# Kernel tuning notes

Hardware: AMD Instinct MI355X
Metric: run time of the kernel (lower is better)

Reference implementation:

```python
import jax, jax.numpy as jnp
import numpy as np

B, S, E, H = 2, 2048, 1024, 16
Dh = E // H
LN_EPS = 1e-5


def setup_inputs() -> dict:
    key = jax.random.key(0)
    ks = jax.random.split(key, 12)
    std = 1.0 / np.sqrt(E)
    inp = {
        "query": jax.random.normal(ks[0], (B, S, E), jnp.float32),
        "key":   jax.random.normal(ks[1], (B, S, E), jnp.float32),
        "value": jax.random.normal(ks[2], (B, S, E), jnp.float32),
        # True = masked. Causal mask so every row keeps >=1 valid entry.
        "mask": jnp.broadcast_to(jnp.triu(jnp.ones((S, S), bool), k=1), (B, S, S)),
        # per-head QKV projections, stacked: weight [H, Dh, E] (torch Linear layout), bias [H, Dh]
        "Wq_w": jax.random.uniform(ks[3], (H, Dh, E), jnp.float32, -std, std),
        "Wq_b": jax.random.uniform(ks[4], (H, Dh), jnp.float32, -std, std),
        "Wk_w": jax.random.uniform(ks[5], (H, Dh, E), jnp.float32, -std, std),
        "Wk_b": jax.random.uniform(ks[6], (H, Dh), jnp.float32, -std, std),
        "Wv_w": jax.random.uniform(ks[7], (H, Dh, E), jnp.float32, -std, std),
        "Wv_b": jax.random.uniform(ks[8], (H, Dh), jnp.float32, -std, std),
        # output projection [E, E] (torch layout: out = x @ W.T + b)
        "out_w": jax.random.uniform(ks[9], (E, E), jnp.float32, -std, std),
        "out_b": jax.random.uniform(ks[10], (E,), jnp.float32, -std, std),
        "ln_g": jnp.ones((E,), jnp.float32),
        "ln_b": jnp.zeros((E,), jnp.float32),
    }
    return inp


def reference(query, key, value, mask, Wq_w, Wq_b, Wk_w, Wk_b, Wv_w, Wv_b, out_w, out_b, ln_g, ln_b):
    # per-head projections (batched over heads): [B,S,E] x [H,Dh,E] -> [B,H,S,Dh]
    q = jnp.einsum('bse,hde->bhsd', query, Wq_w) + Wq_b[None, :, None, :]
    k = jnp.einsum('bse,hde->bhsd', key,   Wk_w) + Wk_b[None, :, None, :]
    v = jnp.einsum('bse,hde->bhsd', value, Wv_w) + Wv_b[None, :, None, :]
    scale = 1.0 / np.sqrt(Dh).astype(np.float32)
    scores = jnp.einsum('bhsd,bhtd->bhst', q, k) * scale  # [B,H,S,S]
    scores = jnp.where(mask[:, None, :, :], -jnp.inf, scores)
    probs = jax.nn.softmax(scores, axis=-1)  # dropout p=0 (eval)
    ctx = jnp.einsum('bhst,bhtd->bhsd', probs, v)  # [B,H,S,Dh]
    att = ctx.transpose(0, 2, 1, 3).reshape(query.shape[0], query.shape[1], -1)  # concat heads [B,S,E]
    proj = att @ out_w.T + out_b  # dropout p=0
    x = query + proj  # residual
    mu = jnp.mean(x, axis=-1, keepdims=True)
    var = jnp.mean(jnp.square(x - mu), axis=-1, keepdims=True)
    return (x - mu) * jax.lax.rsqrt(var + LN_EPS) * ln_g + ln_b
```

## Files before the change

### kernel.cpp

```cpp
#include <hip/hip_runtime.h>
#include <stdint.h>

#define B_ 2
#define S_ 2048
#define E_ 1024
#define H_ 16
#define DH 64
#define M_TOT (B_*S_)

typedef short s16x8 __attribute__((ext_vector_type(8)));
typedef float f32x4 __attribute__((ext_vector_type(4)));
typedef unsigned int u32;
typedef unsigned short u16;

union V8 { uint4 u; s16x8 v; };

__device__ __forceinline__ u32 fbits(float f){ union{float f;u32 i;}x; x.f=f; return x.i; }
__device__ __forceinline__ u32 prround(float f){ return fbits(f)+0x8000u; }
__device__ __forceinline__ u16 f2bf(float f){ return (u16)(prround(f)>>16); }
__device__ __forceinline__ u32 permpack(u32 hi,u32 lo){ return __builtin_amdgcn_perm(hi,lo,0x07060302u); }
__device__ __forceinline__ uint4 pack8r(const float4 a, const float4 b){
    uint4 p;
    p.x = permpack(prround(a.y),prround(a.x));
    p.y = permpack(prround(a.w),prround(a.z));
    p.z = permpack(prround(b.y),prround(b.x));
    p.w = permpack(prround(b.w),prround(b.z));
    return p;
}
__device__ __forceinline__ float exp2_fast(float x){ float r; asm("v_exp_f32 %0, %1":"=v"(r):"v"(x)); return r; }

typedef const __attribute__((address_space(1))) u32* gas_t;
typedef __attribute__((address_space(3))) u32* las_t;
#define GLDS16(gp, lp) __builtin_amdgcn_global_load_lds((gas_t)(gp), (las_t)(lp), 16, 0, 0)

#define MFMA16(a,b,c) __builtin_amdgcn_mfma_f32_16x16x32_bf16((a),(b),(c),0,0,0)

__global__ __launch_bounds__(256) void cvtw(
    const float* __restrict__ w0, const float* __restrict__ w1, const float* __restrict__ w2,
    u16* __restrict__ dst, int n4)
{
    const int z = blockIdx.y;
    const float* s = (z==0)?w0:(z==1)?w1:w2;
    u16* d = dst + (size_t)z*E_*E_;
    int i = blockIdx.x*256 + threadIdx.x;
    const int stride = gridDim.x*256;
    for (; i<n4; i+=stride){
        float4 v = ((const float4*)s)[i];
        uint2 p;
        p.x = permpack(prround(v.y),prround(v.x));
        p.y = permpack(prround(v.w),prround(v.z));
        ((uint2*)d)[i] = p;
    }
}
__global__ __launch_bounds__(256) void cvt1(
    const float* __restrict__ s, u16* __restrict__ d, int n4)
{
    int i = blockIdx.x*256 + threadIdx.x;
    const int stride = gridDim.x*256;
    for (; i<n4; i+=stride){
        float4 v = ((const float4*)s)[i];
        uint2 p;
        p.x = permpack(prround(v.y),prround(v.x));
        p.y = permpack(prround(v.w),prround(v.z));
        ((uint2*)d)[i] = p;
    }
}
__global__ __launch_bounds__(256) void cvtx(
    const float* __restrict__ x0, const float* __restrict__ x1, const float* __restrict__ x2,
    u16* __restrict__ d0, u16* __restrict__ d1, u16* __restrict__ d2, int n4)
{
    const int z = blockIdx.y;
    const float* s = (z==0)?x0:(z==1)?x1:x2;
    u16* d = (z==0)?d0:(z==1)?d1:d2;
    int i = blockIdx.x*256 + threadIdx.x;
    const int stride = gridDim.x*256;
    for (; i<n4; i+=stride){
        float4 v = ((const float4*)s)[i];
        uint2 p;
        p.x = permpack(prround(v.y),prround(v.x));
        p.y = permpack(prround(v.w),prround(v.z));
        ((uint2*)d)[i] = p;
    }
}
__global__ __launch_bounds__(256) void cvtall(
    const float* __restrict__ w0, const float* __restrict__ w1, const float* __restrict__ w2,
    const float* __restrict__ ow,
    const float* __restrict__ x0, const float* __restrict__ x1, const float* __restrict__ x2,
    u16* __restrict__ wbf, u16* __restrict__ owbf,
    u16* __restrict__ dq, u16* __restrict__ dk, u16* __restrict__ dv)
{
    const int z = blockIdx.y;
    const float* s;
    u16* d;
    int n4;
    if (z < 3){ s = (z==0)?w0:(z==1)?w1:w2; d = wbf + (size_t)z*E_*E_; n4 = (E_*E_)/4; }
    else if (z == 3){ s = ow; d = owbf; n4 = (E_*E_)/4; }
    else { s = (z==4)?x0:(z==5)?x1:x2; d = (z==4)?dq:(z==5)?dk:dv; n4 = (M_TOT*E_)/4; }
    int i = blockIdx.x*256 + threadIdx.x;
    const int stride = gridDim.x*256;
    for (; i<n4; i+=stride){
        float4 v = ((const float4*)s)[i];
        uint2 p;
        p.x = permpack(prround(v.y),prround(v.x));
        p.y = permpack(prround(v.w),prround(v.z));
        ((uint2*)d)[i] = p;
    }
}

__global__ __launch_bounds__(256,3) void qkv128(
    const float* __restrict__ xv,
    const u16* __restrict__ xqb, const u16* __restrict__ xkb, const u16* __restrict__ xvb,
    const u16* __restrict__ Wb,
    const float* __restrict__ bq, const float* __restrict__ bk, const float* __restrict__ bv,
    u16* __restrict__ oq, u16* __restrict__ ok_, u16* __restrict__ ovt)
{
    const int bid = blockIdx.x;
    const int c = bid & 7;
    const int tdec = bid >> 3;
    const int n = tdec & 7;
    const int g = ((tdec >> 3) << 3) + c;
    const int m = g & 31, z = g >> 5;

    const u16* W = Wb + (size_t)z*E_*E_;
    const float* bia = (z==0)?bq:(z==1)?bk:bv;
    const float scale = (z==0)? 0.125f*1.44269504f : 1.0f;

    __shared__ __align__(16) u16 As[3][128*32];
    __shared__ __align__(16) u16 Bs[3][128*32];

    const int tid = threadIdx.x;
    const int wid = tid>>6, lane = tid&63;
    const int lrow = lane&15, quad = lane>>4;
    const int mb = m*128, nb = n*128;
    const int wm = (wid>>1)*64, wn = (wid&1)*64;
    const int srow = lane>>2, skq = lane&3;

    f32x4 acc[4][4] = {};
    const u16*  Wn = W + (size_t)nb*E_;

    auto stageB = [&](u16* Bd, int kt){
        const int k0 = kt*32;
#pragma unroll
        for (int i=0;i<2;i++){
            const int rb = wid*32 + i*16;
            GLDS16(Wn + (size_t)(rb+srow)*E_ + k0 + ((skq^(srow&3))<<3), Bd + rb*32);
        }
    };

    const u16* Abf = (z==0)? xqb : (z==1)? xkb : xvb;

    if (Abf){
        const u16* Am = Abf + (size_t)mb*E_;
        auto stageA = [&](u16* Ad, int kt){
            const int k0 = kt*32;
#pragma unroll
            for (int i=0;i<2;i++){
                const int rb = wid*32 + i*16;
                GLDS16(Am + (size_t)(rb+srow)*E_ + k0 + ((skq^(srow&3))<<3), Ad + rb*32);
            }
        };
        stageA(As[0], 0); stageB(Bs[0], 0);
        stageA(As[1], 1); stageB(Bs[1], 1);

        int tc = 0;
#pragma unroll 1
        for (int kt=0; kt<32; ++kt){
            const int ts = (kt+2 < 32) ? kt+2 : 31;
            const int tn = (tc+2 >= 3) ? tc-1 : tc+2;
            asm volatile("s_waitcnt vmcnt(4) lgkmcnt(0)" ::: "memory");
            __builtin_amdgcn_s_barrier();
            __builtin_amdgcn_sched_barrier(0);

            const u16* Ad = As[tc];
            const u16* Bd = Bs[tc];
            const int fq_ = (quad^(lrow&3))<<3;
            s16x8 a0 = *(const s16x8*)&Ad[(wm+ 0+lrow)*32 + fq_];
            s16x8 a1 = *(const s16x8*)&Ad[(wm+16+lrow)*32 + fq_];
            s16x8 a2 = *(const s16x8*)&Ad[(wm+32+lrow)*32 + fq_];
            s16x8 a3 = *(const s16x8*)&Ad[(wm+48+lrow)*32 + fq_];
            s16x8 b0 = *(const s16x8*)&Bd[(wn+ 0+lrow)*32 + fq_];
            s16x8 b1 = *(const s16x8*)&Bd[(wn+16+lrow)*32 + fq_];
            s16x8 b2 = *(const s16x8*)&Bd[(wn+32+lrow)*32 + fq_];
            s16x8 b3 = *(const s16x8*)&Bd[(wn+48+lrow)*32 + fq_];
            __builtin_amdgcn_sched_barrier(0);
            stageA(As[tn], ts);
            stageB(Bs[tn], ts);
            __builtin_amdgcn_sched_barrier(0);
            __builtin_amdgcn_s_setprio(1);
            acc[0][0] = MFMA16(a0, b0, acc[0][0]);
            acc[0][1] = MFMA16(a0, b1, acc[0][1]);
            acc[0][2] = MFMA16(a0, b2, acc[0][2]);
            acc[0][3] = MFMA16(a0, b3, acc[0][3]);
            acc[1][0] = MFMA16(a1, b0, acc[1][0]);
            acc[1][1] = MFMA16(a1, b1, acc[1][1]);
            acc[1][2] = MFMA16(a1, b2, acc[1][2]);
            acc[1][3] = MFMA16(a1, b3, acc[1][3]);
            acc[2][0] = MFMA16(a2, b0, acc[2][0]);
            acc[2][1] = MFMA16(a2, b1, acc[2][1]);
            acc[2][2] = MFMA16(a2, b2, acc[2][2]);
            acc[2][3] = MFMA16(a2, b3, acc[2][3]);
            acc[3][0] = MFMA16(a3, b0, acc[3][0]);
            acc[3][1] = MFMA16(a3, b1, acc[3][1]);
            acc[3][2] = MFMA16(a3, b2, acc[3][2]);
            acc[3][3] = MFMA16(a3, b3, acc[3][3]);
            __builtin_amdgcn_s_setprio(0);
            tc = (tc+1==3)?0:tc+1;
        }
        asm volatile("s_waitcnt vmcnt(0) lgkmcnt(0)" ::: "memory");
    } else {
        const int arow = wid*32 + (lane>>1);
        const int akh  = lane&1;
        const int ag0  = akh*2;
        const int asw  = arow&3;
        const float* Xrow = xv + (size_t)(mb+arow)*E_ + akh*16;

        float4 arA0, arA1, arA2, arA3;
        float4 arB0, arB1, arB2, arB3;

#define QKV_ISSUEA(KT, AR) do {                                   \
        const float* xp_ = Xrow + ((KT)<<5);                      \
        AR##0 = *(const float4*)(xp_    );                        \
        AR##1 = *(const float4*)(xp_ + 4);                        \
        AR##2 = *(const float4*)(xp_ + 8);                        \
        AR##3 = *(const float4*)(xp_ +12);                        \
    } while(0)

#define QKV_WRITEA(AD, AR) do {                                   \
        const uint4 w0_ = pack8r(AR##0, AR##1);                   \
        const uint4 w1_ = pack8r(AR##2, AR##3);                   \
        *(uint4*)&(AD)[arow*32 + (((ag0  )^asw)<<3)] = w0_;       \
        *(uint4*)&(AD)[arow*32 + (((ag0+1)^asw)<<3)] = w1_;       \
    } while(0)

#define QKV_ITER(KT, TC, ARC, ARN) do {                                       \
        const int ts_ = ((KT)+2 < 32) ? (KT)+2 : 31;                          \
        const int tw_ = ((TC)+1==3)?0:(TC)+1;                                 \
        const int tn_ = (tw_+1==3)?0:tw_+1;                                   \
        const u16* Ad_ = As[TC];                                              \
        const u16* Bd_ = Bs[TC];                                              \
        asm volatile("s_waitcnt vmcnt(6) lgkmcnt(0)" ::: "memory");           \
        __builtin_amdgcn_s_barrier();                                         \
        __builtin_amdgcn_sched_barrier(0);                                    \
        const int fq_ = (quad^(lrow&3))<<3;                                   \
        s16x8 a0 = *(const s16x8*)&Ad_[(wm+ 0+lrow)*32 + fq_];                \
        s16x8 a1 = *(const s16x8*)&Ad_[(wm+16+lrow)*32 + fq_];                \
        s16x8 a2 = *(const s16x8*)&Ad_[(wm+32+lrow)*32 + fq_];                \
        s16x8 a3 = *(const s16x8*)&Ad_[(wm+48+lrow)*32 + fq_];                \
        s16x8 b0 = *(const s16x8*)&Bd_[(wn+ 0+lrow)*32 + fq_];                \
        s16x8 b1 = *(const s16x8*)&Bd_[(wn+16+lrow)*32 + fq_];                \
        s16x8 b2 = *(const s16x8*)&Bd_[(wn+32+lrow)*32 + fq_];                \
        s16x8 b3 = *(const s16x8*)&Bd_[(wn+48+lrow)*32 + fq_];                \
        __builtin_amdgcn_sched_barrier(0);                                    \
        QKV_ISSUEA(ts_, ARN);                                                 \
        __builtin_amdgcn_sched_barrier(0);                                    \
        stageB(Bs[tn_], ts_);                                                 \
        __builtin_amdgcn_sched_barrier(0);                                    \
        __builtin_amdgcn_s_setprio(1);                                        \
        acc[0][0] = MFMA16(a0, b0, acc[0][0]);                                \
        acc[0][1] = MFMA16(a0, b1, acc[0][1]);                                \
        acc[0][2] = MFMA16(a0, b2, acc[0][2]);                                \
        acc[0][3] = MFMA16(a0, b3, acc[0][3]);                                \
        acc[1][0] = MFMA16(a1, b0, acc[1][0]);                                \
        acc[1][1] = MFMA16(a1, b1, acc[1][1]);                                \
        acc[1][2] = MFMA16(a1, b2, acc[1][2]);                                \
        acc[1][3] = MFMA16(a1, b3, acc[1][3]);                                \
        __builtin_amdgcn_s_setprio(0);                                        \
        QKV_WRITEA(As[tw_], ARC);                                             \
        __builtin_amdgcn_s_setprio(1);                                        \
        acc[2][0] = MFMA16(a2, b0, acc[2][0]);                                \
        acc[2][1] = MFMA16(a2, b1, acc[2][1]);                                \
        acc[2][2] = MFMA16(a2, b2, acc[2][2]);                                \
        acc[2][3] = MFMA16(a2, b3, acc[2][3]);                                \
        acc[3][0] = MFMA16(a3, b0, acc[3][0]);                                \
        acc[3][1] = MFMA16(a3, b1, acc[3][1]);                                \
        acc[3][2] = MFMA16(a3, b2, acc[3][2]);                                \
        acc[3][3] = MFMA16(a3, b3, acc[3][3]);                                \
        __builtin_amdgcn_s_setprio(0);                                        \
    } while(0)

        QKV_ISSUEA(0, arA);
        stageB(Bs[0], 0);
        QKV_WRITEA(As[0], arA);
        QKV_ISSUEA(1, arA);
        stageB(Bs[1], 1);

        int tc = 0;
#pragma unroll 1
        for (int k2=0; k2<16; ++k2){
            const int kt0 = k2*2;
            QKV_ITER(kt0,   tc, arA, arB);
            tc = (tc+1==3)?0:tc+1;
            QKV_ITER(kt0+1, tc, arB, arA);
            tc = (tc+1==3)?0:tc+1;
        }
        asm volatile("s_waitcnt vmcnt(0) lgkmcnt(0)" ::: "memory");
#undef QKV_ITER
#undef QKV_WRITEA
#undef QKV_ISSUEA
    }

    if (z < 2){
        u16* O = (z==0)?oq:ok_;
#pragma unroll
        for (int ci=0;ci<4;ci++){
            const int nn = nb+wn+ci*16+lrow;
            const float bval = bia[nn];
            const int h = nn>>6, d = nn&63;
#pragma unroll
            for (int mi=0;mi<4;mi++){
#pragma unroll
                for (int r=0;r<4;r++){
                    const int mm = mb+wm+mi*16+quad*4+r;
                    const int bb = mm>>11, s = mm&(S_-1);
                    O[(((size_t)(bb*H_+h))*S_+s)*DH + d] = f2bf((acc[mi][ci][r]+bval)*scale);
                }
            }
        }
    } else {
#pragma unroll
        for (int ci=0;ci<4;ci++){
            const int nn = nb+wn+ci*16+lrow;
            const float bval = bia[nn];
            const int h = nn>>6, d = nn&63;
#pragma unroll
            for (int mi=0;mi<4;mi++){
                const int m0 = mb+wm+mi*16+quad*4;
                const int bb = m0>>11, s0 = m0&(S_-1);
                uint2 pk;
                pk.x = permpack(prround(acc[mi][ci][1]+bval), prround(acc[mi][ci][0]+bval));
                pk.y = permpack(prround(acc[mi][ci][3]+bval), prround(acc[mi][ci][2]+bval));
                *(uint2*)&ovt[(((size_t)(bb*H_+h))*DH + d)*S_ + s0] = pk;
            }
        }
    }
}

__global__ __launch_bounds__(512,2) void attn8(
    const u16* __restrict__ q_ws, const u16* __restrict__ k_ws,
    const u16* __restrict__ vt_ws, u16* __restrict__ att)
{
    const int bid = blockIdx.x;
    const int c8 = bid & 7;
    const int t = bid >> 3;
    const int p = t & 15;
    const int bh = ((t >> 4) << 3) + c8;
    const int b = bh>>4, h = bh&15;

    const u16* Qb = q_ws + (size_t)bh*S_*DH;
    const u16* Kb = k_ws + (size_t)bh*S_*DH;
    const u16* VT = vt_ws + (size_t)bh*DH*S_;

    __shared__ __align__(16) u16 Ks[2][2][64*64];
    __shared__ __align__(16) u16 Vt[2][2][64*64];
    __shared__ __align__(16) u16 Ps[8][16*64];

    const int tid = threadIdx.x;
    const int wid = tid>>6, lane = tid&63;
    const int grp = wid>>2, w4 = wid&3;
    const int lrow = lane&15, quad = lane>>4;
    u16* Pw = Ps[wid];

    const int srw = lane>>3;
    const int scs = lane&7;
    const int sgc = scs ^ srw;

    auto stageKV = [&](u16* Kd, u16* Vd, int t0){
#pragma unroll
        for (int g2=0; g2<2; g2++){
            const int rg = w4*16 + g2*8 + srw;
            GLDS16(Kb + (size_t)(t0+rg)*DH + (sgc<<3), Kd + (w4*16+g2*8)*64);
            GLDS16(VT + (size_t)rg*S_ + t0 + (sgc<<3), Vd + (w4*16+g2*8)*64);
        }
    };

    float* oex = (float*)&Ks[0][0][0];
    float* lex = (float*)&Vt[0][0][0];

    for (int ph=0; ph<2; ph++){
        const int qi = ph ? (31-p) : p;
        const int qb = qi<<6;
        const int ntg   = (qi >= grp) ? (((qi-grp)>>1)+1) : 0;
        const int ntmax = (qi>>1)+1;

        s16x8 qf[2];
#pragma unroll
        for (int ch=0;ch<2;ch++)
            qf[ch] = *(const s16x8*)&Qb[(size_t)(qb+w4*16+lrow)*DH + ch*32 + quad*8];

        f32x4 o[4] = {};
        float l_lane = 0.f;
        const int qglob = qb + w4*16 + lrow;

        auto computeTile = [&](const u16* Kd, const u16* Vd, int t0, bool diag){
            f32x4 st[4] = {};
#pragma unroll
            for (int tt=0;tt<4;tt++){
                const int tr = tt*16+lrow;
#pragma unroll
                for (int ch=0;ch<2;ch++){
                    const int slot = (ch*4+quad) ^ (lrow&7);
                    const s16x8 kf = *(const s16x8*)&Kd[tr*64 + slot*8];
                    st[tt] = __builtin_amdgcn_mfma_f32_16x16x32_bf16(kf, qf[ch], st[tt],0,0,0);
                }
            }
            if (diag){
#pragma unroll
                for (int tt=0;tt<4;tt++){
                    const int tg = t0 + tt*16 + quad*4;
#pragma unroll
                    for (int r=0;r<4;r++)
                        if (tg + r > qglob) st[tt][r] = -1e30f;
                }
            }
#pragma unroll
            for (int tt=0;tt<4;tt++){
                const float p0 = exp2_fast(st[tt][0]);
                const float p1 = exp2_fast(st[tt][1]);
                const float p2 = exp2_fast(st[tt][2]);
                const float p3 = exp2_fast(st[tt][3]);
                l_lane += (p0+p1)+(p2+p3);
                const int tc = tt*2 + (quad>>1);
                const int ts = tc ^ (lrow&7);
                const int a0 = lrow*64 + ts*8 + (quad&1)*4;
                *(u32*)&Pw[a0]   = permpack(prround(p1),prround(p0));
                *(u32*)&Pw[a0+2] = permpack(prround(p3),prround(p2));
            }
            s16x8 pb[2];
#pragma unroll
            for (int ch=0;ch<2;ch++){
                const int slot = (ch*4+quad) ^ (lrow&7);
                pb[ch] = *(const s16x8*)&Pw[lrow*64 + slot*8];
            }
#pragma unroll
            for (int cc=0;cc<4;cc++){
                const int vr = cc*16+lrow;
#pragma unroll
                for (int ch=0;ch<2;ch++){
                    const int slot = (ch*4+quad) ^ (lrow&7);
                    const s16x8 vf = *(const s16x8*)&Vd[vr*64 + slot*8];
                    o[cc] = __builtin_amdgcn_mfma_f32_16x16x32_bf16(vf, pb[ch], o[cc],0,0,0);
                }
            }
        };

        __syncthreads();
        if (ntg > 0) stageKV(Ks[grp][0], Vt[grp][0], grp<<6);
#pragma unroll 1
        for (int i=0; i<ntmax; ++i){
            __syncthreads();
            if (i+1 < ntg) stageKV(Ks[grp][(i+1)&1], Vt[grp][(i+1)&1], (grp+2*(i+1))<<6);
            if (i < ntg){
                const int tile = grp + 2*i;
                computeTile(Ks[grp][i&1], Vt[grp][i&1], tile<<6, tile==qi);
            }
        }

        float s = l_lane;
        s += __shfl_xor(s, 16, 64);
        s += __shfl_xor(s, 32, 64);

        __syncthreads();
        if (grp == 1){
            float* dst = oex + (size_t)(w4*64 + lane)*16;
#pragma unroll
            for (int cc=0;cc<4;cc++) *(f32x4*)&dst[cc*4] = o[cc];
            if (quad == 0) lex[w4*16 + lrow] = s;
        }
        __syncthreads();
        if (grp == 0){
            const float* src = oex + (size_t)(w4*64 + lane)*16;
#pragma unroll
            for (int cc=0;cc<4;cc++) o[cc] += *(const f32x4*)&src[cc*4];
            const float rl = 1.0f/(s + lex[w4*16 + lrow]);
#pragma unroll
            for (int cc=0;cc<4;cc++){
                uint2 pk;
                pk.x = permpack(prround(o[cc][1]*rl), prround(o[cc][0]*rl));
                pk.y = permpack(prround(o[cc][3]*rl), prround(o[cc][2]*rl));
                *(uint2*)&att[(size_t)(b*S_ + qglob)*E_ + h*DH + cc*16 + quad*4] = pk;
            }
        }
    }
}

__global__ __launch_bounds__(256,4) void oproj64(
    const u16* __restrict__ A, const u16* __restrict__ W, const float* __restrict__ bias,
    const float* __restrict__ resid, float* __restrict__ out)
{
    const int bid = blockIdx.x;
    const int c = bid & 7;
    const int tdec = bid >> 3;
    const int n = tdec & 15;
    const int m = ((tdec >> 4) << 3) + c;

    __shared__ __align__(16) u16 As[3][64*32];
    __shared__ __align__(16) u16 Bs[3][64*32];

    const int tid = threadIdx.x;
    const int wid = tid>>6, lane = tid&63;
    const int lrow = lane&15, quad = lane>>4;
    const int mb = m*64, nb = n*64;
    const int wm = (wid>>1)*32, wn = (wid&1)*32;
    const int srow = lane>>2, skq = lane&3;

    f32x4 acc[2][2] = {};
    const u16* Ab = A + (size_t)mb*E_;
    const u16* Wn = W + (size_t)nb*E_;

    auto stage = [&](u16* Ad, u16* Bd, int kt){
        const int k0 = kt*32;
        const int kc = (skq^(srow&3))<<3;
        const int rb = wid*16;
        GLDS16(Ab + (size_t)(rb+srow)*E_ + k0 + kc, Ad + rb*32);
        GLDS16(Wn + (size_t)(rb+srow)*E_ + k0 + kc, Bd + rb*32);
    };

    stage(As[0], Bs[0], 0);
    stage(As[1], Bs[1], 1);

    int tc = 0, tn = 2;
#pragma unroll 1
    for (int kt=0; kt<32; ++kt){
        const int ts = (kt+2 < 32) ? kt+2 : 31;
        asm volatile("s_waitcnt vmcnt(2) lgkmcnt(0)" ::: "memory");
        __builtin_amdgcn_s_barrier();
        __builtin_amdgcn_sched_barrier(0);

        const u16* Ad = As[tc];
        const u16* Bd = Bs[tc];
        const int fq = (quad^(lrow&3))<<3;
        s16x8 a0 = *(const s16x8*)&Ad[(wm+ 0+lrow)*32 + fq];
        s16x8 a1 = *(const s16x8*)&Ad[(wm+16+lrow)*32 + fq];
        s16x8 b0 = *(const s16x8*)&Bd[(wn+ 0+lrow)*32 + fq];
        s16x8 b1 = *(const s16x8*)&Bd[(wn+16+lrow)*32 + fq];
        __builtin_amdgcn_sched_barrier(0);
        stage(As[tn], Bs[tn], ts);
        __builtin_amdgcn_sched_barrier(0);
        __builtin_amdgcn_s_setprio(1);
        acc[0][0] = MFMA16(a0, b0, acc[0][0]);
        acc[0][1] = MFMA16(a0, b1, acc[0][1]);
        acc[1][0] = MFMA16(a1, b0, acc[1][0]);
        acc[1][1] = MFMA16(a1, b1, acc[1][1]);
        __builtin_amdgcn_s_setprio(0);
        tc = (tc+1==3)?0:tc+1;
        tn = (tn+1==3)?0:tn+1;
    }
    asm volatile("s_waitcnt vmcnt(0)" ::: "memory");

#pragma unroll
    for (int ci=0;ci<2;ci++){
        const int nn = nb+wn+ci*16+lrow;
        const float bval = bias[nn];
#pragma unroll
        for (int mi=0;mi<2;mi++){
#pragma unroll
            for (int r=0;r<4;r++){
                const int mm = mb+wm+mi*16+quad*4+r;
                out[(size_t)mm*E_+nn] = acc[mi][ci][r] + bval + resid[(size_t)mm*E_+nn];
            }
        }
    }
}

__global__ __launch_bounds__(256) void ln_k(
    const float* __restrict__ xin, const float* __restrict__ lg,
    const float* __restrict__ lb, float* __restrict__ out)
{
    const int row = blockIdx.x;
    const int tid = threadIdx.x;
    const int wid = tid>>6, lane = tid&63;
    const float* xr = xin + (size_t)row*E_;

    float x[4];
    float s = 0.f;
#pragma unroll
    for (int i=0;i<4;i++){ const int e = i*256+tid; x[i] = xr[e]; s += x[i]; }
    __shared__ float red[8];
#pragma unroll
    for (int off=32; off>0; off>>=1) s += __shfl_xor(s, off, 64);
    if (lane==0) red[wid] = s;
    __syncthreads();
    const float mu = (red[0]+red[1]+red[2]+red[3]) * (1.f/E_);

    float v = 0.f;
#pragma unroll
    for (int i=0;i<4;i++){ const float d = x[i]-mu; v += d*d; }
#pragma unroll
    for (int off=32; off>0; off>>=1) v += __shfl_xor(v, off, 64);
    if (lane==0) red[wid+4] = v;
    __syncthreads();
    const float var = (red[4]+red[5]+red[6]+red[7]) * (1.f/E_);
    const float rs = rsqrtf(var + 1e-5f);

#pragma unroll
    for (int i=0;i<4;i++){
        const int e = i*256+tid;
        out[(size_t)row*E_+e] = (x[i]-mu)*rs*lg[e] + lb[e];
    }
}

extern "C" void kernel_launch(void* const* d_in, const int* in_sizes, int n_in,
                              void* d_out, int out_size, void* d_ws, size_t ws_size,
                              hipStream_t stream) {
    const float* q_in = (const float*)d_in[0];
    const float* k_in = (const float*)d_in[1];
    const float* v_in = (const float*)d_in[2];
    const float* wq = (const float*)d_in[4];
    const float* bq = (const float*)d_in[5];
    const float* wk = (const float*)d_in[6];
    const float* bk = (const float*)d_in[7];
    const float* wv = (const float*)d_in[8];
    const float* bv = (const float*)d_in[9];
    const float* ow = (const float*)d_in[10];
    const float* ob = (const float*)d_in[11];
    const float* lg = (const float*)d_in[12];
    const float* lb = (const float*)d_in[13];
    float* out = (float*)d_out;

    char* ws = (char*)d_ws;
    const size_t MB = (size_t)1<<20;
    u16* q_ws  = (u16*)(ws);
    u16* k_ws  = (u16*)(ws +  8*MB);
    u16* vt_ws = (u16*)(ws + 16*MB);
    u16* att   = (u16*)(ws + 24*MB);
    u16* Wbf   = (u16*)(ws + 24*MB);
    float* proj = (float*)ws;

    u16* xqbf = (u16*)out;
    u16* xkbf = (u16*)((char*)out + 8*MB);

    if (ws_size >= 48*MB){
        u16* xvbf = (u16*)(ws + 32*MB);
        u16* owbf = (u16*)(ws + 40*MB);

        cvtall<<<dim3(1024,7), 256, 0, stream>>>(
            wq, wk, wv, ow, q_in, k_in, v_in, Wbf, owbf, xqbf, xkbf, xvbf);
        qkv128<<<dim3(768), 256, 0, stream>>>(
            v_in, xqbf, xkbf, xvbf, Wbf, bq, bk, bv, q_ws, k_ws, vt_ws);
        attn8<<<dim3(512), 512, 0, stream>>>(q_ws, k_ws, vt_ws, att);
        oproj64<<<dim3(1024), 256, 0, stream>>>(att, owbf, ob, q_in, proj);
        ln_k<<<dim3(M_TOT), 256, 0, stream>>>(proj, lg, lb, out);
    } else {
        u16* owbf = (u16*)(ws + 16*MB);
        u16* xvbf = (ws_size >= 40*MB) ? (u16*)(ws + 32*MB) : (u16*)0;

        cvtw<<<dim3(512,3), 256, 0, stream>>>(wq, wk, wv, Wbf, (E_*E_)/4);
        cvtx<<<dim3(1024, xvbf?3:2), 256, 0, stream>>>(
            q_in, k_in, v_in, xqbf, xkbf, xvbf, (M_TOT*E_)/4);
        qkv128<<<dim3(768), 256, 0, stream>>>(
            v_in, xqbf, xkbf, xvbf, Wbf, bq, bk, bv, q_ws, k_ws, vt_ws);
        attn8<<<dim3(512), 512, 0, stream>>>(q_ws, k_ws, vt_ws, att);
        cvt1<<<dim3(1024), 256, 0, stream>>>(ow, owbf, (E_*E_)/4);
        oproj64<<<dim3(1024), 256, 0, stream>>>(att, owbf, ob, q_in, proj);
        ln_k<<<dim3(M_TOT), 256, 0, stream>>>(proj, lg, lb, out);
    }
}
```

Baseline: 234.8 us.

## Use 128x128 split-K output projection and fold bias/residual into LayerNorm

Replaces the 64x64-tile output projection with a 128x128-tile kernel that splits K into two halves, writing two fp32 partial sums to separate buffers. A new LayerNorm kernel adds the two partials, the output bias and the residual before normalizing. The larger tiles raise data reuse per block while split-K keeps the grid at 512 blocks. The cost is extra fp32 partial traffic, a larger workspace requirement (64MB), and falling back to the old path when the workspace is smaller.

```diff
diff --git a/kernel.cpp b/kernel.cpp
--- a/kernel.cpp
+++ b/kernel.cpp
@@ -483,6 +483,112 @@
     }
 }
 
+__global__ __launch_bounds__(256,3) void oproj_ks(
+    const u16* __restrict__ A, const u16* __restrict__ W,
+    float* __restrict__ p0, float* __restrict__ p1)
+{
+    const int bid = blockIdx.x;
+    const int c = bid & 7;
+    const int tdec = bid >> 3;
+    const int n = tdec & 7;
+    const int g = ((tdec >> 3) << 3) + c;
+    const int m = g & 31, half = g >> 5;
+
+    __shared__ __align__(16) u16 As[3][128*32];
+    __shared__ __align__(16) u16 Bs[3][128*32];
+
+    const int tid = threadIdx.x;
+    const int wid = tid>>6, lane = tid&63;
+    const int lrow = lane&15, quad = lane>>4;
+    const int mb = m*128, nb = n*128;
+    const int wm = (wid>>1)*64, wn = (wid&1)*64;
+    const int srow = lane>>2, skq = lane&3;
+
+    f32x4 acc[4][4] = {};
+    const u16* Am = A + (size_t)mb*E_ + half*512;
+    const u16* Wn = W + (size_t)nb*E_ + half*512;
+    float* P = half ? p1 : p0;
+
+    auto stageA = [&](u16* Ad, int kt){
+        const int k0 = kt*32;
+#pragma unroll
+        for (int i=0;i<2;i++){
+            const int rb = wid*32 + i*16;
+            GLDS16(Am + (size_t)(rb+srow)*E_ + k0 + ((skq^(srow&3))<<3), Ad + rb*32);
+        }
+    };
+    auto stageB = [&](u16* Bd, int kt){
+        const int k0 = kt*32;
+#pragma unroll
+        for (int i=0;i<2;i++){
+            const int rb = wid*32 + i*16;
+            GLDS16(Wn + (size_t)(rb+srow)*E_ + k0 + ((skq^(srow&3))<<3), Bd + rb*32);
+        }
+    };
+
+    stageA(As[0], 0); stageB(Bs[0], 0);
+    stageA(As[1], 1); stageB(Bs[1], 1);
+
+    int tc = 0;
+#pragma unroll 1
+    for (int kt=0; kt<16; ++kt){
+        const int ts = (kt+2 < 16) ? kt+2 : 15;
+        const int tn = (tc+2 >= 3) ? tc-1 : tc+2;
+        asm volatile("s_waitcnt vmcnt(4) lgkmcnt(0)" ::: "memory");
+        __builtin_amdgcn_s_barrier();
+        __builtin_amdgcn_sched_barrier(0);
+
+        const u16* Ad = As[tc];
+        const u16* Bd = Bs[tc];
+        const int fq_ = (quad^(lrow&3))<<3;
+        s16x8 a0 = *(const s16x8*)&Ad[(wm+ 0+lrow)*32 + fq_];
+        s16x8 a1 = *(const s16x8*)&Ad[(wm+16+lrow)*32 + fq_];
+        s16x8 a2 = *(const s16x8*)&Ad[(wm+32+lrow)*32 + fq_];
+        s16x8 a3 = *(const s16x8*)&Ad[(wm+48+lrow)*32 + fq_];
+        s16x8 b0 = *(const s16x8*)&Bd[(wn+ 0+lrow)*32 + fq_];
+        s16x8 b1 = *(const s16x8*)&Bd[(wn+16+lrow)*32 + fq_];
+        s16x8 b2 = *(const s16x8*)&Bd[(wn+32+lrow)*32 + fq_];
+        s16x8 b3 = *(const s16x8*)&Bd[(wn+48+lrow)*32 + fq_];
+        __builtin_amdgcn_sched_barrier(0);
+        stageA(As[tn], ts);
+        stageB(Bs[tn], ts);
+        __builtin_amdgcn_sched_barrier(0);
+        __builtin_amdgcn_s_setprio(1);
+        acc[0][0] = MFMA16(a0, b0, acc[0][0]);
+        acc[0][1] = MFMA16(a0, b1, acc[0][1]);
+        acc[0][2] = MFMA16(a0, b2, acc[0][2]);
+        acc[0][3] = MFMA16(a0, b3, acc[0][3]);
+        acc[1][0] = MFMA16(a1, b0, acc[1][0]);
+        acc[1][1] = MFMA16(a1, b1, acc[1][1]);
+        acc[1][2] = MFMA16(a1, b2, acc[1][2]);
+        acc[1][3] = MFMA16(a1, b3, acc[1][3]);
+        acc[2][0] = MFMA16(a2, b0, acc[2][0]);
+        acc[2][1] = MFMA16(a2, b1, acc[2][1]);
+        acc[2][2] = MFMA16(a2, b2, acc[2][2]);
+        acc[2][3] = MFMA16(a2, b3, acc[2][3]);
+        acc[3][0] = MFMA16(a3, b0, acc[3][0]);
+        acc[3][1] = MFMA16(a3, b1, acc[3][1]);
+        acc[3][2] = MFMA16(a3, b2, acc[3][2]);
+        acc[3][3] = MFMA16(a3, b3, acc[3][3]);
+        __builtin_amdgcn_s_setprio(0);
+        tc = (tc+1==3)?0:tc+1;
+    }
+    asm volatile("s_waitcnt vmcnt(0) lgkmcnt(0)" ::: "memory");
+
+#pragma unroll
+    for (int ci=0;ci<4;ci++){
+        const int nn = nb+wn+ci*16+lrow;
+#pragma unroll
+        for (int mi=0;mi<4;mi++){
+#pragma unroll
+            for (int r=0;r<4;r++){
+                const int mm = mb+wm+mi*16+quad*4+r;
+                P[(size_t)mm*E_+nn] = acc[mi][ci][r];
+            }
+        }
+    }
+}
+
 __global__ __launch_bounds__(256,4) void oproj64(
     const u16* __restrict__ A, const u16* __restrict__ W, const float* __restrict__ bias,
     const float* __restrict__ resid, float* __restrict__ out)
@@ -598,6 +704,48 @@
         out[(size_t)row*E_+e] = (x[i]-mu)*rs*lg[e] + lb[e];
     }
 }
+__global__ __launch_bounds__(256) void ln2_k(
+    const float* __restrict__ p0, const float* __restrict__ p1,
+    const float* __restrict__ ob, const float* __restrict__ resid,
+    const float* __restrict__ lg, const float* __restrict__ lb,
+    float* __restrict__ out)
+{
+    const int row = blockIdx.x;
+    const int tid = threadIdx.x;
+    const int wid = tid>>6, lane = tid&63;
+    const size_t base = (size_t)row*E_;
+
+    float x[4];
+    float s = 0.f;
+#pragma unroll
+    for (int i=0;i<4;i++){
+        const int e = i*256+tid;
+        x[i] = p0[base+e] + p1[base+e] + ob[e] + resid[base+e];
+        s += x[i];
+    }
+    __shared__ float red[8];
+#pragma unroll
+    for (int off=32; off>0; off>>=1) s += __shfl_xor(s, off, 64);
+    if (lane==0) red[wid] = s;
+    __syncthreads();
+    const float mu = (red[0]+red[1]+red[2]+red[3]) * (1.f/E_);
+
+    float v = 0.f;
+#pragma unroll
+    for (int i=0;i<4;i++){ const float d = x[i]-mu; v += d*d; }
+#pragma unroll
+    for (int off=32; off>0; off>>=1) v += __shfl_xor(v, off, 64);
+    if (lane==0) red[wid+4] = v;
+    __syncthreads();
+    const float var = (red[4]+red[5]+red[6]+red[7]) * (1.f/E_);
+    const float rs = rsqrtf(var + 1e-5f);
+
+#pragma unroll
+    for (int i=0;i<4;i++){
+        const int e = i*256+tid;
+        out[base+e] = (x[i]-mu)*rs*lg[e] + lb[e];
+    }
+}
 
 extern "C" void kernel_launch(void* const* d_in, const int* in_sizes, int n_in,
                               void* d_out, int out_size, void* d_ws, size_t ws_size,
@@ -629,17 +777,18 @@
     u16* xqbf = (u16*)out;
     u16* xkbf = (u16*)((char*)out + 8*MB);
 
-    if (ws_size >= 48*MB){
-        u16* xvbf = (u16*)(ws + 32*MB);
-        u16* owbf = (u16*)(ws + 40*MB);
+    if (ws_size >= 64*MB){
+        u16*   xvbf  = (u16*)(ws + 32*MB);
+        u16*   owbf  = (u16*)(ws + 40*MB);
+        float* proj1 = (float*)(ws + 48*MB);
 
         cvtall<<<dim3(1024,7), 256, 0, stream>>>(
             wq, wk, wv, ow, q_in, k_in, v_in, Wbf, owbf, xqbf, xkbf, xvbf);
         qkv128<<<dim3(768), 256, 0, stream>>>(
             v_in, xqbf, xkbf, xvbf, Wbf, bq, bk, bv, q_ws, k_ws, vt_ws);
         attn8<<<dim3(512), 512, 0, stream>>>(q_ws, k_ws, vt_ws, att);
-        oproj64<<<dim3(1024), 256, 0, stream>>>(att, owbf, ob, q_in, proj);
-        ln_k<<<dim3(M_TOT), 256, 0, stream>>>(proj, lg, lb, out);
+        oproj_ks<<<dim3(512), 256, 0, stream>>>(att, owbf, proj, proj1);
+        ln2_k<<<dim3(M_TOT), 256, 0, stream>>>(proj, proj1, ob, q_in, lg, lb, out);
     } else {
         u16* owbf = (u16*)(ws + 16*MB);
         u16* xvbf = (ws_size >= 40*MB) ? (u16*)(ws + 32*MB) : (u16*)0;
```

Result: no change. 239.4 us (+2.0%).
